# Kernel optimization log

Hardware: AMD Instinct MI355X
Metric: run time of the kernel (lower is better)

The kernel has to match this reference:

```python
import jax, jax.numpy as jnp
import numpy as np

# SLAYER neuron params (from network.yaml defaults)
THETA = 10.0      # spike threshold
TAU_SR = 10.0     # synaptic (PSP) time constant
TAU_REF = 1.0     # refractory time constant
SCALE_REF = 2.0   # refractory strength (in units of theta)
TAU_RHO = 1.0     # surrogate-gradient width
SCALE_RHO = 1.0   # surrogate-gradient scale
TS = 1.0          # simulation timestep


@jax.custom_vjp
def spike_heaviside(u):
    # SLAYER spike generation: hard threshold in forward
    return (u >= THETA).astype(u.dtype)

def _spk_fwd(u):
    return spike_heaviside(u), u

def _spk_bwd(u, g):
    # SLAYER surrogate: rho(u) = (scaleRho/tauRho) * exp(-|u - theta| / tauRho)
    surr = (SCALE_RHO / TAU_RHO) * jnp.exp(-jnp.abs(u - THETA) / TAU_RHO)
    return (g * surr,)

spike_heaviside.defvjp(_spk_fwd, _spk_bwd)


def psp(x):
    """Temporal post-synaptic-potential filter (exponential synapse kernel).
    x: (B, T, F) -> (B, T, F);  p[t] = decay * p[t-1] + x[t]."""
    decay = jnp.exp(jnp.asarray(-TS / TAU_SR, x.dtype))
    def step(p, xt):
        p = decay * p + xt
        return p, p
    p0 = jnp.zeros((x.shape[0], x.shape[2]), x.dtype)
    _, ps = jax.lax.scan(step, p0, jnp.swapaxes(x, 0, 1))  # scan over T
    return jnp.swapaxes(ps, 0, 1)


def spike(u):
    """Thresholded spike generation with refractory feedback.
    u: (B, T, F) membrane input; refractory state subtracts 2*theta after a spike
    and decays with tauRef (SLAYER refractory response)."""
    decay_ref = jnp.exp(jnp.asarray(-TS / TAU_REF, u.dtype))
    def step(r, ut):
        v = ut + r
        s = spike_heaviside(v)
        r = decay_ref * (r - SCALE_REF * THETA * s)
        return r, s
    r0 = jnp.zeros((u.shape[0], u.shape[2]), u.dtype)
    _, ss = jax.lax.scan(step, r0, jnp.swapaxes(u, 0, 1))  # scan over T
    return jnp.swapaxes(ss, 0, 1)


def setup_inputs() -> dict:
    key = jax.random.key(0)
    k1, k2, k3 = jax.random.split(key, 3)
    B, T, F_IN, F_H, F_OUT = 64, 500, 1250, 512, 2
    x = (jax.random.uniform(k1, (B, T, F_IN)) < 0.1).astype(jnp.float32)
    W1 = jax.random.normal(k2, (F_H, F_IN), jnp.float32) * 0.05
    W2 = jax.random.normal(k3, (F_OUT, F_H), jnp.float32) * 0.05
    return {"x": x, "W1": W1, "W2": W2}


def reference(x, W1, W2):
    # layer 1: dense projection per timestep -> PSP filter -> spike
    s1 = spike(psp(jnp.einsum('btf,hf->bth', x, W1)))   # (B, T, 512)
    # layer 2
    out = spike(psp(jnp.einsum('bth,oh->bto', s1, W2))) # (B, T, 2)
    return out
```

## Files before the change

kernel.cpp:

```cpp
#include <hip/hip_runtime.h>
#include <hip/hip_bf16.h>
#include <cstdint>
#include <cstddef>

#define B_N   64
#define T_N   500
#define K_IN  1250
#define KP    1280
#define N_H   512
#define M_N   32000

#define BM 64
#define BK 32
#define NT (KP / BK)

typedef __attribute__((ext_vector_type(8))) short bf16x8;
typedef __attribute__((ext_vector_type(4))) float f32x4;

#define DECAY_SR  0.9048374180359595732f
#define DECAY_REF 0.3678794411714423216f
#define THETA 10.0f

__device__ __forceinline__ unsigned short f2bf(float f) {
  __hip_bfloat16 h = __float2bfloat16(f);
  return *reinterpret_cast<unsigned short*>(&h);
}
__device__ __forceinline__ uint32_t f2bf2(float a, float b) {
  float2 t; t.x = a; t.y = b;
  __hip_bfloat162 h = __float22bfloat162_rn(t);
  return *reinterpret_cast<uint32_t*>(&h);
}
__device__ __forceinline__ float bf2f(unsigned short s) {
  union { uint32_t u; float f; } v; v.u = ((uint32_t)s) << 16; return v.f;
}

__global__ __launch_bounds__(256) void w1cvt_kernel(const float* __restrict__ W1,
                                                    short* __restrict__ W1b) {
  int k = blockIdx.x * 256 + threadIdx.x;
  int n = blockIdx.y;
  float v = (k < K_IN) ? W1[(size_t)n * K_IN + k] : 0.f;
  W1b[(size_t)n * KP + k] = (short)f2bf(v);
}

__global__ __launch_bounds__(256) void gemm1_kernel(const float* __restrict__ X,
                                                    const short* __restrict__ W1b,
                                                    unsigned short* __restrict__ U1) {
  __shared__ short As[2][BM * BK];
  __shared__ short Bs[2][N_H * BK];
  const int tid  = threadIdx.x;
  const int bm   = blockIdx.x * BM;
  const int w    = tid >> 6;
  const int lane = tid & 63;
  const int lrow = lane & 15;
  const int lgrp = lane >> 4;
  const int lsw  = lgrp ^ ((lrow >> 1) & 3);

  f32x4 acc[4][8];
  #pragma unroll
  for (int i = 0; i < 4; ++i)
    #pragma unroll
    for (int j = 0; j < 8; ++j)
      acc[i][j] = (f32x4){0.f, 0.f, 0.f, 0.f};

  const int arow  = tid >> 2;
  const int aslot = tid & 3;
  const int awofs = arow * BK + ((aslot ^ ((arow >> 1) & 3)) * 8);
  const int brow16 = lane >> 2;
  const int bslp   = lane & 3;

  auto stage = [&](int buf, int k0) {
    #pragma unroll
    for (int c = 0; c < 8; ++c) {
      int n  = w * 128 + c * 16 + brow16;
      int ss = bslp ^ ((n >> 1) & 3);
      const short* src = W1b + (size_t)n * KP + k0 + ss * 8;
      __builtin_amdgcn_global_load_lds(
          (const __attribute__((address_space(1))) void*)src,
          (__attribute__((address_space(3))) void*)&Bs[buf][(w * 128 + c * 16) * BK],
          16, 0, 0);
    }
    {
      int gk = k0 + aslot * 8;
      const float* s = X + (size_t)(bm + arow) * K_IN + gk;
      float v0, v1, v2, v3, v4, v5, v6, v7;
      if (gk + 7 < K_IN) {
        float2 x0 = *(const float2*)(s);
        float2 x1 = *(const float2*)(s + 2);
        float2 x2 = *(const float2*)(s + 4);
        float2 x3 = *(const float2*)(s + 6);
        v0 = x0.x; v1 = x0.y; v2 = x1.x; v3 = x1.y;
        v4 = x2.x; v5 = x2.y; v6 = x3.x; v7 = x3.y;
      } else {
        v0 = (gk + 0 < K_IN) ? s[0] : 0.f;
        v1 = (gk + 1 < K_IN) ? s[1] : 0.f;
        v2 = (gk + 2 < K_IN) ? s[2] : 0.f;
        v3 = (gk + 3 < K_IN) ? s[3] : 0.f;
        v4 = (gk + 4 < K_IN) ? s[4] : 0.f;
        v5 = (gk + 5 < K_IN) ? s[5] : 0.f;
        v6 = (gk + 6 < K_IN) ? s[6] : 0.f;
        v7 = (gk + 7 < K_IN) ? s[7] : 0.f;
      }
      uint4 pk;
      pk.x = f2bf2(v0, v1); pk.y = f2bf2(v2, v3);
      pk.z = f2bf2(v4, v5); pk.w = f2bf2(v6, v7);
      *(uint4*)&As[buf][awofs] = pk;
    }
  };

  stage(0, 0);
  __syncthreads();
  int pb = 0;
  for (int t = 0; t < NT; ++t) {
    if (t + 1 < NT) stage(pb ^ 1, (t + 1) * BK);
    bf16x8 af[4], bv[8];
    #pragma unroll
    for (int i = 0; i < 4; ++i)
      af[i] = *(const bf16x8*)&As[pb][(i * 16 + lrow) * BK + lsw * 8];
    #pragma unroll
    for (int j = 0; j < 8; ++j)
      bv[j] = *(const bf16x8*)&Bs[pb][(w * 128 + j * 16 + lrow) * BK + lsw * 8];
    #pragma unroll
    for (int i = 0; i < 4; ++i)
      #pragma unroll
      for (int j = 0; j < 8; ++j)
        acc[i][j] = __builtin_amdgcn_mfma_f32_16x16x32_bf16(af[i], bv[j], acc[i][j], 0, 0, 0);
    __syncthreads();
    pb ^= 1;
  }

  #pragma unroll
  for (int i = 0; i < 4; ++i) {
    int row0 = bm + i * 16 + lgrp * 4;
    #pragma unroll
    for (int j = 0; j < 8; ++j) {
      int col = w * 128 + j * 16 + lrow;
      #pragma unroll
      for (int r = 0; r < 4; ++r)
        U1[(size_t)(row0 + r) * N_H + col] = f2bf(acc[i][j][r]);
    }
  }
}

__global__ __launch_bounds__(128) void scan1_kernel(const unsigned short* __restrict__ U1,
                                                    unsigned long long* __restrict__ S1m) {
  int idx  = blockIdx.x * 128 + threadIdx.x;
  int b    = idx >> 9, h = idx & 511;
  int lane = threadIdx.x & 63;
  const unsigned short* u = U1 + (size_t)b * T_N * N_H + h;
  unsigned long long* mout = S1m + (size_t)b * T_N * 8 + (h >> 6);
  float p = 0.f, r = 0.f;
  float bufA[10], bufB[10];

  auto load = [&](float* buf, int t0) {
    #pragma unroll
    for (int j = 0; j < 10; ++j) buf[j] = bf2f(u[(size_t)(t0 + j) * N_H]);
  };
  auto proc = [&](const float* buf, int t0) {
    #pragma unroll
    for (int j = 0; j < 10; ++j) {
      p = DECAY_SR * p + buf[j];
      float v = p + r;
      bool sp = (v >= THETA);
      r = DECAY_REF * (r - (sp ? 2.f * THETA : 0.f));
      unsigned long long bal = __ballot(sp);
      if (lane == 0) mout[(size_t)(t0 + j) * 8] = bal;
    }
  };

  load(bufA, 0);
  for (int g = 0; g < 25; ++g) {
    int ta = g * 20, tb = ta + 10;
    load(bufB, tb);
    proc(bufA, ta);
    if (g < 24) load(bufA, tb + 10);
    proc(bufB, tb);
  }
}

__global__ __launch_bounds__(256) void gemm2_kernel(const unsigned char* __restrict__ S1b,
                                                    const float* __restrict__ W2,
                                                    float* __restrict__ U2) {
  int m    = blockIdx.x * 4 + (threadIdx.x >> 6);
  int lane = threadIdx.x & 63;
  unsigned int byte = S1b[(size_t)m * 64 + lane];
  float a0 = 0.f, a1 = 0.f;
  #pragma unroll
  for (int j = 0; j < 8; ++j) {
    int h = lane * 8 + j;
    float sel = ((byte >> j) & 1u) ? 1.f : 0.f;
    a0 += sel * W2[h];
    a1 += sel * W2[N_H + h];
  }
  #pragma unroll
  for (int off = 32; off >= 1; off >>= 1) {
    a0 += __shfl_down(a0, off);
    a1 += __shfl_down(a1, off);
  }
  if (lane == 0) {
    U2[(size_t)m * 2]     = a0;
    U2[(size_t)m * 2 + 1] = a1;
  }
}

__global__ __launch_bounds__(128) void scan2_kernel(const float* __restrict__ U2,
                                                    float* __restrict__ OUT) {
  __shared__ float lu[T_N * 2];
  __shared__ float ls[T_N * 2];
  int b = blockIdx.x;
  const float* src = U2 + (size_t)b * T_N * 2;
  for (int i = threadIdx.x; i < T_N * 2; i += 128) lu[i] = src[i];
  __syncthreads();
  if (threadIdx.x < 2) {
    int o = threadIdx.x;
    float p = 0.f, r = 0.f;
    for (int t = 0; t < T_N; ++t) {
      p = DECAY_SR * p + lu[t * 2 + o];
      float v = p + r;
      float sp = (v >= THETA) ? 1.f : 0.f;
      r = DECAY_REF * (r - 2.f * THETA * sp);
      ls[t * 2 + o] = sp;
    }
  }
  __syncthreads();
  float* dst = OUT + (size_t)b * T_N * 2;
  for (int i = threadIdx.x; i < T_N * 2; i += 128) dst[i] = ls[i];
}

extern "C" void kernel_launch(void* const* d_in, const int* in_sizes, int n_in,
                              void* d_out, int out_size, void* d_ws, size_t ws_size,
                              hipStream_t stream) {
  const float* X  = (const float*)d_in[0];
  const float* W1 = (const float*)d_in[1];
  const float* W2 = (const float*)d_in[2];
  float* OUT = (float*)d_out;

  char* ws = (char*)d_ws;
  short*              W1b = (short*)ws;
  unsigned short*     U1  = (unsigned short*)(ws + 1310720);
  unsigned long long* S1m = (unsigned long long*)(ws + 34078720);
  float*              U2  = (float*)(ws + 36126720);

  w1cvt_kernel<<<dim3(KP / 256, N_H), 256, 0, stream>>>(W1, W1b);
  gemm1_kernel<<<dim3(M_N / BM), 256, 0, stream>>>(X, W1b, U1);
  scan1_kernel<<<dim3((B_N * N_H) / 128), 128, 0, stream>>>(U1, S1m);
  gemm2_kernel<<<dim3(M_N / 4), 256, 0, stream>>>((const unsigned char*)S1m, W2, U2);
  scan2_kernel<<<dim3(B_N), 128, 0, stream>>>(U2, OUT);
}
```

Before: 382.0 us.

## Bit-pack binary spike input and expand via LDS LUT in GEMM1

Adds a pre-pass that packs the fp32 input X into one bit per element using wave ballots. GEMM1 then reads one byte per 8 K-elements and expands it to bf16 fragments through a 256-entry shared-memory lookup table. This replaces the large fp32 X reads and per-tile conversions, and the GEMM tiling moves to 128x256 tiles on a 2D grid. It assumes the input is exactly 0 or 1 (thresholded at 0.5), which holds for spike inputs but adds an extra kernel launch and a full pass over X.

Measured after the change: 362.9 us. 5.0% less time.

```diff
diff --git a/kernel.cpp b/kernel.cpp
--- a/kernel.cpp
+++ b/kernel.cpp
@@ -10,9 +10,11 @@
 #define N_H   512
 #define M_N   32000
 
-#define BM 64
+#define BM 128
+#define BN 256
 #define BK 32
 #define NT (KP / BK)
+#define XROWB (KP / 8)
 
 typedef __attribute__((ext_vector_type(8))) short bf16x8;
 typedef __attribute__((ext_vector_type(4))) float f32x4;
@@ -25,13 +27,23 @@
   __hip_bfloat16 h = __float2bfloat16(f);
   return *reinterpret_cast<unsigned short*>(&h);
 }
-__device__ __forceinline__ uint32_t f2bf2(float a, float b) {
-  float2 t; t.x = a; t.y = b;
-  __hip_bfloat162 h = __float22bfloat162_rn(t);
-  return *reinterpret_cast<uint32_t*>(&h);
-}
 __device__ __forceinline__ float bf2f(unsigned short s) {
   union { uint32_t u; float f; } v; v.u = ((uint32_t)s) << 16; return v.f;
+}
+
+__global__ __launch_bounds__(256) void xpack_kernel(const float* __restrict__ X,
+                                                    unsigned long long* __restrict__ Xb64) {
+  int gw   = (blockIdx.x * 256 + threadIdx.x) >> 6;
+  int lane = threadIdx.x & 63;
+  const float* xr = X + (size_t)gw * K_IN;
+  unsigned long long* out = Xb64 + (size_t)gw * (XROWB / 8);
+  #pragma unroll
+  for (int wd = 0; wd < 20; ++wd) {
+    int k = wd * 64 + lane;
+    float v = (k < K_IN) ? xr[k] : 0.f;
+    unsigned long long m = __ballot(v > 0.5f);
+    if (lane == 0) out[wd] = m;
+  }
 }
 
 __global__ __launch_bounds__(256) void w1cvt_kernel(const float* __restrict__ W1,
@@ -42,19 +54,32 @@
   W1b[(size_t)n * KP + k] = (short)f2bf(v);
 }
 
-__global__ __launch_bounds__(256) void gemm1_kernel(const float* __restrict__ X,
+__global__ __launch_bounds__(256) void gemm1_kernel(const unsigned char* __restrict__ Xb,
                                                     const short* __restrict__ W1b,
                                                     unsigned short* __restrict__ U1) {
-  __shared__ short As[2][BM * BK];
-  __shared__ short Bs[2][N_H * BK];
+  __shared__ short Bs[2][BN * BK];
+  __shared__ short LUT[256 * 8];
   const int tid  = threadIdx.x;
-  const int bm   = blockIdx.x * BM;
+  const int bn   = blockIdx.x * BN;
+  const int bm   = blockIdx.y * BM;
   const int w    = tid >> 6;
   const int lane = tid & 63;
+  const int wr   = w >> 1;
+  const int wc   = w & 1;
   const int lrow = lane & 15;
   const int lgrp = lane >> 4;
   const int lsw  = lgrp ^ ((lrow >> 1) & 3);
 
+  {
+    int b = tid;
+    uint32_t w0 = ((b & 1)  ? 0x3F80u : 0u) | ((b & 2)  ? 0x3F800000u : 0u);
+    uint32_t w1 = ((b & 4)  ? 0x3F80u : 0u) | ((b & 8)  ? 0x3F800000u : 0u);
+    uint32_t w2 = ((b & 16) ? 0x3F80u : 0u) | ((b & 32) ? 0x3F800000u : 0u);
+    uint32_t w3 = ((b & 64) ? 0x3F80u : 0u) | ((b & 128)? 0x3F800000u : 0u);
+    uint4 q; q.x = w0; q.y = w1; q.z = w2; q.w = w3;
+    *(uint4*)&LUT[b * 8] = q;
+  }
+
   f32x4 acc[4][8];
   #pragma unroll
   for (int i = 0; i < 4; ++i)
@@ -62,63 +87,52 @@
     for (int j = 0; j < 8; ++j)
       acc[i][j] = (f32x4){0.f, 0.f, 0.f, 0.f};
 
-  const int arow  = tid >> 2;
-  const int aslot = tid & 3;
-  const int awofs = arow * BK + ((aslot ^ ((arow >> 1) & 3)) * 8);
   const int brow16 = lane >> 2;
   const int bslp   = lane & 3;
-
-  auto stage = [&](int buf, int k0) {
-    #pragma unroll
-    for (int c = 0; c < 8; ++c) {
-      int n  = w * 128 + c * 16 + brow16;
-      int ss = bslp ^ ((n >> 1) & 3);
-      const short* src = W1b + (size_t)n * KP + k0 + ss * 8;
+  const unsigned char* xb0 = Xb + (size_t)(bm + wr * 64 + lrow) * XROWB + lgrp;
+
+  auto stageB = [&](int buf, int k0) {
+    #pragma unroll
+    for (int c = 0; c < 4; ++c) {
+      int ch = w * 4 + c;
+      int nl = ch * 16 + brow16;
+      int ss = bslp ^ ((nl >> 1) & 3);
+      const short* src = W1b + (size_t)(bn + nl) * KP + k0 + ss * 8;
       __builtin_amdgcn_global_load_lds(
           (const __attribute__((address_space(1))) void*)src,
-          (__attribute__((address_space(3))) void*)&Bs[buf][(w * 128 + c * 16) * BK],
-          16, 0, 0);
-    }
-    {
-      int gk = k0 + aslot * 8;
-      const float* s = X + (size_t)(bm + arow) * K_IN + gk;
-      float v0, v1, v2, v3, v4, v5, v6, v7;
-      if (gk + 7 < K_IN) {
-        float2 x0 = *(const float2*)(s);
-        float2 x1 = *(const float2*)(s + 2);
-        float2 x2 = *(const float2*)(s + 4);
-        float2 x3 = *(const float2*)(s + 6);
-        v0 = x0.x; v1 = x0.y; v2 = x1.x; v3 = x1.y;
-        v4 = x2.x; v5 = x2.y; v6 = x3.x; v7 = x3.y;
-      } else {
-        v0 = (gk + 0 < K_IN) ? s[0] : 0.f;
-        v1 = (gk + 1 < K_IN) ? s[1] : 0.f;
-        v2 = (gk + 2 < K_IN) ? s[2] : 0.f;
-        v3 = (gk + 3 < K_IN) ? s[3] : 0.f;
-        v4 = (gk + 4 < K_IN) ? s[4] : 0.f;
-        v5 = (gk + 5 < K_IN) ? s[5] : 0.f;
-        v6 = (gk + 6 < K_IN) ? s[6] : 0.f;
-        v7 = (gk + 7 < K_IN) ? s[7] : 0.f;
-      }
-      uint4 pk;
-      pk.x = f2bf2(v0, v1); pk.y = f2bf2(v2, v3);
-      pk.z = f2bf2(v4, v5); pk.w = f2bf2(v6, v7);
-      *(uint4*)&As[buf][awofs] = pk;
+          (__attribute__((address_space(3))) void*)&Bs[buf][ch * 16 * BK], 16, 0, 0);
     }
   };
 
-  stage(0, 0);
+  stageB(0, 0);
+  unsigned char c0 = xb0[0];
+  unsigned char c1 = xb0[16 * XROWB];
+  unsigned char c2 = xb0[32 * XROWB];
+  unsigned char c3 = xb0[48 * XROWB];
   __syncthreads();
+
   int pb = 0;
   for (int t = 0; t < NT; ++t) {
-    if (t + 1 < NT) stage(pb ^ 1, (t + 1) * BK);
-    bf16x8 af[4], bv[8];
-    #pragma unroll
-    for (int i = 0; i < 4; ++i)
-      af[i] = *(const bf16x8*)&As[pb][(i * 16 + lrow) * BK + lsw * 8];
-    #pragma unroll
-    for (int j = 0; j < 8; ++j)
-      bv[j] = *(const bf16x8*)&Bs[pb][(w * 128 + j * 16 + lrow) * BK + lsw * 8];
+    unsigned char n0 = c0, n1 = c1, n2 = c2, n3 = c3;
+    if (t + 1 < NT) {
+      stageB(pb ^ 1, (t + 1) * BK);
+      const unsigned char* xbn = xb0 + (t + 1) * 4;
+      n0 = xbn[0];
+      n1 = xbn[16 * XROWB];
+      n2 = xbn[32 * XROWB];
+      n3 = xbn[48 * XROWB];
+    }
+    bf16x8 af[4];
+    af[0] = *(const bf16x8*)&LUT[(int)c0 * 8];
+    af[1] = *(const bf16x8*)&LUT[(int)c1 * 8];
+    af[2] = *(const bf16x8*)&LUT[(int)c2 * 8];
+    af[3] = *(const bf16x8*)&LUT[(int)c3 * 8];
+    bf16x8 bv[8];
+    #pragma unroll
+    for (int j = 0; j < 8; ++j) {
+      int r = wc * 128 + j * 16 + lrow;
+      bv[j] = *(const bf16x8*)&Bs[pb][r * BK + lsw * 8];
+    }
     #pragma unroll
     for (int i = 0; i < 4; ++i)
       #pragma unroll
@@ -126,14 +140,15 @@
         acc[i][j] = __builtin_amdgcn_mfma_f32_16x16x32_bf16(af[i], bv[j], acc[i][j], 0, 0, 0);
     __syncthreads();
     pb ^= 1;
+    c0 = n0; c1 = n1; c2 = n2; c3 = n3;
   }
 
   #pragma unroll
   for (int i = 0; i < 4; ++i) {
-    int row0 = bm + i * 16 + lgrp * 4;
+    int row0 = bm + wr * 64 + i * 16 + lgrp * 4;
     #pragma unroll
     for (int j = 0; j < 8; ++j) {
-      int col = w * 128 + j * 16 + lrow;
+      int col = bn + wc * 128 + j * 16 + lrow;
       #pragma unroll
       for (int r = 0; r < 4; ++r)
         U1[(size_t)(row0 + r) * N_H + col] = f2bf(acc[i][j][r]);
@@ -239,9 +254,11 @@
   unsigned short*     U1  = (unsigned short*)(ws + 1310720);
   unsigned long long* S1m = (unsigned long long*)(ws + 34078720);
   float*              U2  = (float*)(ws + 36126720);
-
-  w1cvt_kernel<<<dim3(KP / 256, N_H), 256, 0, stream>>>(W1, W1b);
-  gemm1_kernel<<<dim3(M_N / BM), 256, 0, stream>>>(X, W1b, U1);
+  unsigned long long* Xb  = (unsigned long long*)(ws + 36382720);
+
+  xpack_kernel<<<dim3(M_N / 4), 256, 0, stream>>>(X, Xb);
+  w1cvt_kernel<<<dim3(KP / 256, N_H), 256, 0, stream>>>(W1, (short*)W1b);
+  gemm1_kernel<<<dim3(N_H / BN, M_N / BM), 256, 0, stream>>>((const unsigned char*)Xb, W1b, U1);
   scan1_kernel<<<dim3((B_N * N_H) / 128), 128, 0, stream>>>(U1, S1m);
   gemm2_kernel<<<dim3(M_N / 4), 256, 0, stream>>>((const unsigned char*)S1m, W2, U2);
   scan2_kernel<<<dim3(B_N), 128, 0, stream>>>(U2, OUT);
```
